# Optimization experiments

Hardware: AMD Instinct MI355X
Metric: run time of the kernel (lower is better)

## Reference

```python
import jax, jax.numpy as jnp
import numpy as np
import math

B, T, C = 4, 2048, 1024
N_HEAD = 16


def setup_inputs() -> dict:
    key = jax.random.key(0)
    ks = jax.random.split(key, 5)
    s = 0.02
    return {
        "x": jax.random.normal(ks[0], (B, T, C), jnp.float32),
        "W_attn": jax.random.normal(ks[1], (C, 3 * C), jnp.float32) * s,
        "b_attn": jax.random.normal(ks[2], (3 * C,), jnp.float32) * s,
        "W_proj": jax.random.normal(ks[3], (C, C), jnp.float32) * s,
        "b_proj": jax.random.normal(ks[4], (C,), jnp.float32) * s,
    }


def reference(x, W_attn, b_attn, W_proj, b_proj):
    b, t, c = x.shape
    hd = c // N_HEAD  # head dim
    qkv = x @ W_attn + b_attn                       # [B,T,3C]
    q, k, v = jnp.split(qkv, 3, axis=-1)
    # [B,T,C] -> [B,H,T,hd]
    q = q.reshape(b, t, N_HEAD, hd).transpose(0, 2, 1, 3)
    k = k.reshape(b, t, N_HEAD, hd).transpose(0, 2, 1, 3)
    v = v.reshape(b, t, N_HEAD, hd).transpose(0, 2, 1, 3)
    att = jnp.einsum("bhqd,bhkd->bhqk", q, k) * (1.0 / math.sqrt(hd))
    causal = jnp.tril(jnp.ones((t, t), dtype=bool))
    att = jnp.where(causal, att, -jnp.inf)
    att = jax.nn.softmax(att, axis=-1)              # dropout disabled (eval mode)
    y = jnp.einsum("bhqk,bhkd->bhqd", att, v)       # [B,H,T,hd]
    y = y.transpose(0, 2, 1, 3).reshape(b, t, c)
    out = y @ W_proj + b_proj                       # resid dropout disabled (eval)
    return out
```

## Files before the change

kernel.cpp:

```cpp
#include <hip/hip_runtime.h>

#define B_  4
#define T_  2048
#define C_  1024
#define H_  16
#define D_  64
#define BT_ 8192

typedef __bf16 bf16x8 __attribute__((ext_vector_type(8)));
typedef float  f32x4  __attribute__((ext_vector_type(4)));

#define MFMA(a, b, c) __builtin_amdgcn_mfma_f32_16x16x32_bf16((a), (b), (c), 0, 0, 0)
#define LOG2E 1.4426950408889634f

__device__ __forceinline__ float fexp2(float x) {
#if __has_builtin(__builtin_amdgcn_exp2f)
    return __builtin_amdgcn_exp2f(x);
#else
    return __expf(x * 0.6931471805599453f);
#endif
}

__device__ __forceinline__ unsigned short f2bf(float f) {
    union { float f; unsigned u; } v; v.f = f;
    unsigned r = v.u + 0x7FFFu + ((v.u >> 16) & 1u);
    return (unsigned short)(r >> 16);
}

__device__ __forceinline__ void gll16(const unsigned short* g, unsigned short* l) {
    __builtin_amdgcn_global_load_lds((const __attribute__((address_space(1))) void*)g,
                                     (__attribute__((address_space(3))) void*)l, 16, 0, 0);
}

template <int GPR>
__device__ __forceinline__ void stage16(const unsigned short* grow0, size_t stride_us,
                                        unsigned short* lds, int chunk) {
    const int lane = threadIdx.x & 63;
    const int gidx = chunk * 64 + lane;
    const int row  = gidx / GPR, c = gidx % GPR;
    const int csrc = c ^ (row & (GPR - 1));
    gll16(grow0 + (size_t)row * stride_us + csrc * 8, lds + gidx * 8);
}

__global__ __launch_bounds__(256) void convert_bf16_kernel(const float* __restrict__ in,
                                                           unsigned short* __restrict__ out) {
    int i = (blockIdx.x * 256 + threadIdx.x) * 4;
    float4 v = *(const float4*)&in[i];
    ushort4 o;
    o.x = f2bf(v.x); o.y = f2bf(v.y); o.z = f2bf(v.z); o.w = f2bf(v.w);
    *(ushort4*)&out[i] = o;
}

__global__ __launch_bounds__(256) void transpose_bf16_kernel(const float* __restrict__ in,
                                                             unsigned short* __restrict__ out,
                                                             int K, int N) {
    __shared__ float tile[32][33];
    int n0 = blockIdx.x * 32, k0 = blockIdx.y * 32;
    int tr = threadIdx.x >> 3, tc = (threadIdx.x & 7) * 4;
    float4 v = *(const float4*)&in[(size_t)(k0 + tr) * N + n0 + tc];
    tile[tr][tc + 0] = v.x; tile[tr][tc + 1] = v.y;
    tile[tr][tc + 2] = v.z; tile[tr][tc + 3] = v.w;
    __syncthreads();
    ushort4 o;
    o.x = f2bf(tile[tc + 0][tr]);
    o.y = f2bf(tile[tc + 1][tr]);
    o.z = f2bf(tile[tc + 2][tr]);
    o.w = f2bf(tile[tc + 3][tr]);
    *(ushort4*)&out[(size_t)(n0 + tr) * K + k0 + tc] = o;
}

__global__ __launch_bounds__(256) void transpose_v_kernel(const unsigned short* __restrict__ qkv,
                                                          unsigned short* __restrict__ vT) {
    __shared__ unsigned short tile[64][65];
    const int bh = blockIdx.y;
    const int b = bh >> 4, h = bh & 15;
    const int t0 = blockIdx.x * 64;
    const size_t src = (size_t)b * 2048 * 3072 + 2048 + h * 64;
    const size_t dbase = (size_t)bh * (T_ * D_);
    const int r = threadIdx.x >> 2, c = (threadIdx.x & 3) * 16;
    uint4 a0 = *(const uint4*)&qkv[src + (size_t)(t0 + r) * 3072 + c];
    uint4 a1 = *(const uint4*)&qkv[src + (size_t)(t0 + r) * 3072 + c + 8];
    const unsigned short* ap = (const unsigned short*)&a0;
    #pragma unroll
    for (int i = 0; i < 8; ++i) tile[r][c + i] = ap[i];
    ap = (const unsigned short*)&a1;
    #pragma unroll
    for (int i = 0; i < 8; ++i) tile[r][c + 8 + i] = ap[i];
    __syncthreads();
    unsigned short tmp[16];
    #pragma unroll
    for (int i = 0; i < 16; ++i) tmp[i] = tile[c + i][r];
    *(uint4*)&vT[dbase + (size_t)r * T_ + t0 + c]     = *(uint4*)&tmp[0];
    *(uint4*)&vT[dbase + (size_t)r * T_ + t0 + c + 8] = *(uint4*)&tmp[8];
}

template <int MODE>
__global__ __launch_bounds__(256) void gemm_bf16_kernel(
    const unsigned short* __restrict__ A,
    const unsigned short* __restrict__ Bt,
    const float* __restrict__ bias,
    float* __restrict__ outF,
    unsigned short* __restrict__ outB,
    int M, int N, int K)
{
    __shared__ __align__(16) unsigned short smem[8192];
    unsigned short* As = smem;
    unsigned short* Bs = smem + 4096;
    const int tid = threadIdx.x;
    const int wave = tid >> 6, lane = tid & 63;
    const int wr = wave >> 1, wc = wave & 1;
    const int g = lane >> 4, li = lane & 15;
    const int m0 = blockIdx.y * 128, n0 = blockIdx.x * 128;

    f32x4 acc[4][4] = {};

    for (int k0 = 0; k0 < K; k0 += 32) {
        __syncthreads();
        stage16<4>(A  + (size_t)m0 * K + k0, K, As, wave * 2);
        stage16<4>(A  + (size_t)m0 * K + k0, K, As, wave * 2 + 1);
        stage16<4>(Bt + (size_t)n0 * K + k0, K, Bs, wave * 2);
        stage16<4>(Bt + (size_t)n0 * K + k0, K, Bs, wave * 2 + 1);
        __syncthreads();
        bf16x8 af[4], bfr[4];
        #pragma unroll
        for (int mi = 0; mi < 4; ++mi) {
            const int row = wr * 64 + mi * 16 + li;
            af[mi] = *(const bf16x8*)&As[row * 32 + ((g ^ (row & 3)) * 8)];
        }
        #pragma unroll
        for (int ni = 0; ni < 4; ++ni) {
            const int row = wc * 64 + ni * 16 + li;
            bfr[ni] = *(const bf16x8*)&Bs[row * 32 + ((g ^ (row & 3)) * 8)];
        }
        #pragma unroll
        for (int mi = 0; mi < 4; ++mi)
            #pragma unroll
            for (int ni = 0; ni < 4; ++ni)
                acc[mi][ni] = MFMA(af[mi], bfr[ni], acc[mi][ni]);
    }

    float bb[4];
    #pragma unroll
    for (int ni = 0; ni < 4; ++ni) bb[ni] = bias[n0 + wc * 64 + ni * 16 + li];

    if (MODE == 0) {
        __syncthreads();
        unsigned short* stg = smem + wave * 1152;
        const float qsc = (n0 < 1024) ? 0.125f * LOG2E : 1.0f;
        const int srow = lane & 15, scp = lane >> 4;
        #pragma unroll
        for (int mi = 0; mi < 4; ++mi) {
            #pragma unroll
            for (int ni = 0; ni < 4; ++ni)
                #pragma unroll
                for (int r = 0; r < 4; ++r)
                    stg[(g * 4 + r) * 72 + ni * 16 + li] = f2bf((acc[mi][ni][r] + bb[ni]) * qsc);
            __builtin_amdgcn_wave_barrier();
            uint4 w0 = *(const uint4*)&stg[srow * 72 + scp * 16];
            uint4 w1 = *(const uint4*)&stg[srow * 72 + scp * 16 + 8];
            unsigned short* dst = &outB[(size_t)(m0 + wr * 64 + mi * 16 + srow) * N
                                        + n0 + wc * 64 + scp * 16];
            *(uint4*)dst = w0;
            *(uint4*)&dst[8] = w1;
            __builtin_amdgcn_wave_barrier();
        }
    } else {
        #pragma unroll
        for (int mi = 0; mi < 4; ++mi)
            #pragma unroll
            for (int ni = 0; ni < 4; ++ni) {
                const int col = n0 + wc * 64 + ni * 16 + li;
                #pragma unroll
                for (int r = 0; r < 4; ++r)
                    outF[(size_t)(m0 + wr * 64 + mi * 16 + g * 4 + r) * N + col]
                        = acc[mi][ni][r] + bb[ni];
            }
    }
}

__global__ __launch_bounds__(256, 4) void flash_attn_kernel(
    const unsigned short* __restrict__ qkv,
    const unsigned short* __restrict__ vT,
    unsigned short* __restrict__ y)
{
    __shared__ __align__(16) unsigned short Ks[64 * 64];
    __shared__ __align__(16) unsigned short Vt[64 * 64];
    __shared__ __align__(16) unsigned short Pq[4][2][16][40];
    const int tid = threadIdx.x;
    const int wv = tid >> 6, lane = tid & 63;
    const int g = lane >> 4, li = lane & 15;
    const int bid = blockIdx.x;
    const int xcd = bid & 7, i = bid >> 3;
    const int bh = xcd * 8 + (i & 7);
    const int p  = i >> 3;
    const int qtA = p, qtB = 31 - p;
    const int b = bh >> 4, h = bh & 15;
    const size_t qrowbase = (size_t)b * 2048 * 3072 + h * 64;
    const size_t vbase = (size_t)bh * (D_ * T_);
    const unsigned short* kbase = qkv + qrowbase + 1024;

    const int rowA = qtA * 64 + wv * 16 + li;
    const int rowB = qtB * 64 + wv * 16 + li;

    bf16x8 aqA[2], aqB[2];
    #pragma unroll
    for (int kc = 0; kc < 2; ++kc) {
        aqA[kc] = *(const bf16x8*)&qkv[qrowbase + (size_t)rowA * 3072 + kc * 32 + g * 8];
        aqB[kc] = *(const bf16x8*)&qkv[qrowbase + (size_t)rowB * 3072 + kc * 32 + g * 8];
    }

    f32x4 oA[4] = {}, oB[4] = {};
    float lA = 0.f, lB = 0.f;
    const float OFS = 8.0f * LOG2E;

    const int nkb = qtB + 1;

    for (int kb = 0; kb < nkb; ++kb) {
        const int k0 = kb << 6;
        __syncthreads();
        stage16<8>(kbase + (size_t)k0 * 3072, 3072, Ks, wv * 2);
        stage16<8>(kbase + (size_t)k0 * 3072, 3072, Ks, wv * 2 + 1);
        stage16<8>(vT + vbase + k0, T_, Vt, wv * 2);
        stage16<8>(vT + vbase + k0, T_, Vt, wv * 2 + 1);
        __syncthreads();
        const bool doA = (kb <= qtA);

        #pragma unroll
        for (int half = 0; half < 2; ++half) {
            f32x4 sA[2], sB[2];
            #pragma unroll
            for (int t2 = 0; t2 < 2; ++t2) {
                const int krow = (half * 2 + t2) * 16 + li;
                bf16x8 ka0 = *(const bf16x8*)&Ks[krow * 64 + ((g       ^ (krow & 7)) * 8)];
                bf16x8 ka1 = *(const bf16x8*)&Ks[krow * 64 + (((4 + g) ^ (krow & 7)) * 8)];
                f32x4 z = {};
                z = MFMA(ka0, aqB[0], z);
                sB[t2] = MFMA(ka1, aqB[1], z);
                if (doA) {
                    f32x4 z2 = {};
                    z2 = MFMA(ka0, aqA[0], z2);
                    sA[t2] = MFMA(ka1, aqA[1], z2);
                }
            }
            #pragma unroll
            for (int t2 = 0; t2 < 2; ++t2) {
                const int kkb = k0 + (half * 2 + t2) * 16;
                {
                    const bool diag = (kb == qtB);
                    ushort4 pw;
                    #pragma unroll
                    for (int r = 0; r < 4; ++r) {
                        float sv = sB[t2][r];
                        if (diag && (kkb + g * 4 + r > rowB)) sv = -1e30f;
                        float pp = fexp2(sv - OFS);
                        lB += pp;
                        ((unsigned short*)&pw)[r] = f2bf(pp);
                    }
                    *(ushort4*)&Pq[wv][1][li][t2 * 16 + g * 4] = pw;
                }
                if (doA) {
                    const bool diag = (kb == qtA);
                    ushort4 pw;
                    #pragma unroll
                    for (int r = 0; r < 4; ++r) {
                        float sv = sA[t2][r];
                        if (diag && (kkb + g * 4 + r > rowA)) sv = -1e30f;
                        float pp = fexp2(sv - OFS);
                        lA += pp;
                        ((unsigned short*)&pw)[r] = f2bf(pp);
                    }
                    *(ushort4*)&Pq[wv][0][li][t2 * 16 + g * 4] = pw;
                }
            }
            __builtin_amdgcn_wave_barrier();
            bf16x8 bpB = *(const bf16x8*)&Pq[wv][1][li][g * 8];
            bf16x8 bpA;
            if (doA) bpA = *(const bf16x8*)&Pq[wv][0][li][g * 8];
            #pragma unroll
            for (int ot = 0; ot < 4; ++ot) {
                const int vrow = ot * 16 + li;
                bf16x8 av = *(const bf16x8*)&Vt[vrow * 64 + (((half * 4 + g) ^ (vrow & 7)) * 8)];
                oB[ot] = MFMA(av, bpB, oB[ot]);
                if (doA) oA[ot] = MFMA(av, bpA, oA[ot]);
            }
            __builtin_amdgcn_wave_barrier();
        }
    }

    #pragma unroll
    for (int t = 0; t < 2; ++t) {
        float l = t ? lB : lA;
        const f32x4* o = t ? oB : oA;
        l += __shfl_xor(l, 16, 64);
        l += __shfl_xor(l, 32, 64);
        float inv = 1.f / l;
        const int trow = (t ? rowB : rowA);
        const size_t yrow = ((size_t)(b * 2048 + trow)) * 1024 + h * 64;
        #pragma unroll
        for (int ot = 0; ot < 4; ++ot) {
            ushort4 pw;
            #pragma unroll
            for (int r = 0; r < 4; ++r)
                ((unsigned short*)&pw)[r] = f2bf(o[ot][r] * inv);
            *(ushort4*)&y[yrow + ot * 16 + g * 4] = pw;
        }
    }
}

extern "C" void kernel_launch(void* const* d_in, const int* in_sizes, int n_in,
                              void* d_out, int out_size, void* d_ws, size_t ws_size,
                              hipStream_t stream)
{
    const float* x      = (const float*)d_in[0];
    const float* W_attn = (const float*)d_in[1];
    const float* b_attn = (const float*)d_in[2];
    const float* W_proj = (const float*)d_in[3];
    const float* b_proj = (const float*)d_in[4];
    float* out = (float*)d_out;

    char* ws = (char*)d_ws;
    size_t off = 0;
    auto alloc = [&](size_t bytes) -> void* {
        void* p = ws + off;
        off += (bytes + 255) & ~(size_t)255;
        return p;
    };
    unsigned short* xb   = (unsigned short*)alloc((size_t)BT_ * C_ * 2);
    unsigned short* Wab  = (unsigned short*)alloc((size_t)3 * C_ * C_ * 2);
    unsigned short* Wpb  = (unsigned short*)alloc((size_t)C_ * C_ * 2);
    unsigned short* qkvb = (unsigned short*)alloc((size_t)BT_ * 3 * C_ * 2);
    unsigned short* yb   = (unsigned short*)alloc((size_t)BT_ * C_ * 2);

    convert_bf16_kernel<<<(BT_ * C_) / 1024, 256, 0, stream>>>(x, xb);
    transpose_bf16_kernel<<<dim3(3 * C_ / 32, C_ / 32), 256, 0, stream>>>(W_attn, Wab, C_, 3 * C_);
    transpose_bf16_kernel<<<dim3(C_ / 32, C_ / 32), 256, 0, stream>>>(W_proj, Wpb, C_, C_);

    gemm_bf16_kernel<0><<<dim3(3 * C_ / 128, BT_ / 128), 256, 0, stream>>>(
        xb, Wab, b_attn, nullptr, qkvb, BT_, 3 * C_, C_);

    unsigned short* vTb = xb;
    transpose_v_kernel<<<dim3(T_ / 64, B_ * H_), 256, 0, stream>>>(qkvb, vTb);

    flash_attn_kernel<<<1024, 256, 0, stream>>>(qkvb, vTb, yb);

    gemm_bf16_kernel<1><<<dim3(C_ / 128, BT_ / 128), 256, 0, stream>>>(
        yb, Wpb, b_proj, out, nullptr, BT_, C_, C_);
}
```

Measured before the change: 279.9 us.

## Fuse prep kernels, write V transposed from QKV GEMM, double-buffer flash K/V

Merges the x conversion and both weight transposes into one launch. The QKV GEMM epilogue now writes V directly in transposed layout when the workspace has room, which removes the separate V-transpose kernel. The flash attention kernel double-buffers its K/V tiles in LDS so the next block's loads overlap the current block's compute, and it shares one P staging buffer between the two query tiles. The trade-offs are more LDS per block, which may reduce occupancy, and extra barriers in the P path.

```diff
diff --git a/kernel.cpp b/kernel.cpp
--- a/kernel.cpp
+++ b/kernel.cpp
@@ -42,21 +42,27 @@
     gll16(grow0 + (size_t)row * stride_us + csrc * 8, lds + gidx * 8);
 }
 
-__global__ __launch_bounds__(256) void convert_bf16_kernel(const float* __restrict__ in,
-                                                           unsigned short* __restrict__ out) {
-    int i = (blockIdx.x * 256 + threadIdx.x) * 4;
-    float4 v = *(const float4*)&in[i];
-    ushort4 o;
-    o.x = f2bf(v.x); o.y = f2bf(v.y); o.z = f2bf(v.z); o.w = f2bf(v.w);
-    *(ushort4*)&out[i] = o;
-}
-
-__global__ __launch_bounds__(256) void transpose_bf16_kernel(const float* __restrict__ in,
-                                                             unsigned short* __restrict__ out,
-                                                             int K, int N) {
+__global__ __launch_bounds__(256) void prep_kernel(const float* __restrict__ x,
+                                                   unsigned short* __restrict__ xb,
+                                                   const float* __restrict__ Wa,
+                                                   unsigned short* __restrict__ Wab,
+                                                   const float* __restrict__ Wp,
+                                                   unsigned short* __restrict__ Wpb) {
     __shared__ float tile[32][33];
-    int n0 = blockIdx.x * 32, k0 = blockIdx.y * 32;
-    int tr = threadIdx.x >> 3, tc = (threadIdx.x & 7) * 4;
+    const int bid = blockIdx.x;
+    if (bid < 8192) {
+        int i = bid * 1024 + threadIdx.x * 4;
+        float4 v = *(const float4*)&x[i];
+        ushort4 o;
+        o.x = f2bf(v.x); o.y = f2bf(v.y); o.z = f2bf(v.z); o.w = f2bf(v.w);
+        *(ushort4*)&xb[i] = o;
+        return;
+    }
+    const float* in; unsigned short* out; int N, t;
+    if (bid < 11264) { t = bid - 8192;  in = Wa; out = Wab; N = 3072; }
+    else             { t = bid - 11264; in = Wp; out = Wpb; N = 1024; }
+    const int n0 = (t % (N / 32)) * 32, k0 = (t / (N / 32)) * 32;
+    const int tr = threadIdx.x >> 3, tc = (threadIdx.x & 7) * 4;
     float4 v = *(const float4*)&in[(size_t)(k0 + tr) * N + n0 + tc];
     tile[tr][tc + 0] = v.x; tile[tr][tc + 1] = v.y;
     tile[tr][tc + 2] = v.z; tile[tr][tc + 3] = v.w;
@@ -66,7 +72,7 @@
     o.y = f2bf(tile[tc + 1][tr]);
     o.z = f2bf(tile[tc + 2][tr]);
     o.w = f2bf(tile[tc + 3][tr]);
-    *(ushort4*)&out[(size_t)(n0 + tr) * K + k0 + tc] = o;
+    *(ushort4*)&out[(size_t)(n0 + tr) * 1024 + k0 + tc] = o;
 }
 
 __global__ __launch_bounds__(256) void transpose_v_kernel(const unsigned short* __restrict__ qkv,
@@ -94,16 +100,17 @@
     *(uint4*)&vT[dbase + (size_t)r * T_ + t0 + c + 8] = *(uint4*)&tmp[8];
 }
 
-template <int MODE>
+template <int MODE, int VDIRECT>
 __global__ __launch_bounds__(256) void gemm_bf16_kernel(
     const unsigned short* __restrict__ A,
     const unsigned short* __restrict__ Bt,
     const float* __restrict__ bias,
     float* __restrict__ outF,
     unsigned short* __restrict__ outB,
+    unsigned short* __restrict__ vTout,
     int M, int N, int K)
 {
-    __shared__ __align__(16) unsigned short smem[8192];
+    __shared__ __align__(16) unsigned short smem[(MODE == 0 && VDIRECT) ? 10240 : 8192];
     unsigned short* As = smem;
     unsigned short* Bs = smem + 4096;
     const int tid = threadIdx.x;
@@ -145,24 +152,54 @@
 
     if (MODE == 0) {
         __syncthreads();
-        unsigned short* stg = smem + wave * 1152;
-        const float qsc = (n0 < 1024) ? 0.125f * LOG2E : 1.0f;
-        const int srow = lane & 15, scp = lane >> 4;
-        #pragma unroll
-        for (int mi = 0; mi < 4; ++mi) {
-            #pragma unroll
-            for (int ni = 0; ni < 4; ++ni)
+        if (VDIRECT && n0 >= 2048) {
+            const int h = (n0 - 2048 + wc * 64) >> 6;
+            const int b = m0 >> 11;
+            const int tb = (m0 & 2047) + wr * 64;
+            unsigned short* vstg = smem + wave * 2560;
+            #pragma unroll
+            for (int mp = 0; mp < 2; ++mp) {
                 #pragma unroll
-                for (int r = 0; r < 4; ++r)
-                    stg[(g * 4 + r) * 72 + ni * 16 + li] = f2bf((acc[mi][ni][r] + bb[ni]) * qsc);
-            __builtin_amdgcn_wave_barrier();
-            uint4 w0 = *(const uint4*)&stg[srow * 72 + scp * 16];
-            uint4 w1 = *(const uint4*)&stg[srow * 72 + scp * 16 + 8];
-            unsigned short* dst = &outB[(size_t)(m0 + wr * 64 + mi * 16 + srow) * N
-                                        + n0 + wc * 64 + scp * 16];
-            *(uint4*)dst = w0;
-            *(uint4*)&dst[8] = w1;
-            __builtin_amdgcn_wave_barrier();
+                for (int mh = 0; mh < 2; ++mh) {
+                    const int mi = mp * 2 + mh;
+                    #pragma unroll
+                    for (int ni = 0; ni < 4; ++ni)
+                        #pragma unroll
+                        for (int r = 0; r < 4; ++r)
+                            vstg[(ni * 16 + li) * 40 + mh * 16 + g * 4 + r]
+                                = f2bf(acc[mi][ni][r] + bb[ni]);
+                }
+                __builtin_amdgcn_wave_barrier();
+                uint4 w0 = *(const uint4*)&vstg[lane * 40];
+                uint4 w1 = *(const uint4*)&vstg[lane * 40 + 8];
+                uint4 w2 = *(const uint4*)&vstg[lane * 40 + 16];
+                uint4 w3 = *(const uint4*)&vstg[lane * 40 + 24];
+                unsigned short* dp = vTout
+                    + (((size_t)(b * 16 + h) * 64 + lane) * 2048 + tb + mp * 32);
+                *(uint4*)dp = w0; *(uint4*)&dp[8] = w1;
+                *(uint4*)&dp[16] = w2; *(uint4*)&dp[24] = w3;
+                __builtin_amdgcn_wave_barrier();
+            }
+        } else {
+            unsigned short* stg = smem + wave * 1152;
+            const float qsc = (n0 < 1024) ? 0.125f * LOG2E : 1.0f;
+            const int srow = lane & 15, scp = lane >> 4;
+            #pragma unroll
+            for (int mi = 0; mi < 4; ++mi) {
+                #pragma unroll
+                for (int ni = 0; ni < 4; ++ni)
+                    #pragma unroll
+                    for (int r = 0; r < 4; ++r)
+                        stg[(g * 4 + r) * 72 + ni * 16 + li] = f2bf((acc[mi][ni][r] + bb[ni]) * qsc);
+                __builtin_amdgcn_wave_barrier();
+                uint4 w0 = *(const uint4*)&stg[srow * 72 + scp * 16];
+                uint4 w1 = *(const uint4*)&stg[srow * 72 + scp * 16 + 8];
+                unsigned short* dst = &outB[(size_t)(m0 + wr * 64 + mi * 16 + srow) * N
+                                            + n0 + wc * 64 + scp * 16];
+                *(uint4*)dst = w0;
+                *(uint4*)&dst[8] = w1;
+                __builtin_amdgcn_wave_barrier();
+            }
         }
     } else {
         #pragma unroll
@@ -183,9 +220,9 @@
     const unsigned short* __restrict__ vT,
     unsigned short* __restrict__ y)
 {
-    __shared__ __align__(16) unsigned short Ks[64 * 64];
-    __shared__ __align__(16) unsigned short Vt[64 * 64];
-    __shared__ __align__(16) unsigned short Pq[4][2][16][40];
+    __shared__ __align__(16) unsigned short Ks[2][64 * 64];
+    __shared__ __align__(16) unsigned short Vt[2][64 * 64];
+    __shared__ __align__(16) unsigned short Pq[4][16][40];
     const int tid = threadIdx.x;
     const int wv = tid >> 6, lane = tid & 63;
     const int g = lane >> 4, li = lane & 15;
@@ -212,18 +249,28 @@
     f32x4 oA[4] = {}, oB[4] = {};
     float lA = 0.f, lB = 0.f;
     const float OFS = 8.0f * LOG2E;
-
     const int nkb = qtB + 1;
 
+    stage16<8>(kbase, 3072, Ks[0], wv * 2);
+    stage16<8>(kbase, 3072, Ks[0], wv * 2 + 1);
+    stage16<8>(vT + vbase, T_, Vt[0], wv * 2);
+    stage16<8>(vT + vbase, T_, Vt[0], wv * 2 + 1);
+
     for (int kb = 0; kb < nkb; ++kb) {
+        const int cur = kb & 1;
+        __syncthreads();
+        if (kb + 1 < nkb) {
+            const int kn = (kb + 1) << 6;
+            const int nxt = cur ^ 1;
+            stage16<8>(kbase + (size_t)kn * 3072, 3072, Ks[nxt], wv * 2);
+            stage16<8>(kbase + (size_t)kn * 3072, 3072, Ks[nxt], wv * 2 + 1);
+            stage16<8>(vT + vbase + kn, T_, Vt[nxt], wv * 2);
+            stage16<8>(vT + vbase + kn, T_, Vt[nxt], wv * 2 + 1);
+        }
         const int k0 = kb << 6;
-        __syncthreads();
-        stage16<8>(kbase + (size_t)k0 * 3072, 3072, Ks, wv * 2);
-        stage16<8>(kbase + (size_t)k0 * 3072, 3072, Ks, wv * 2 + 1);
-        stage16<8>(vT + vbase + k0, T_, Vt, wv * 2);
-        stage16<8>(vT + vbase + k0, T_, Vt, wv * 2 + 1);
-        __syncthreads();
         const bool doA = (kb <= qtA);
+        const unsigned short* ksb = Ks[cur];
+        const unsigned short* vtb = Vt[cur];
 
         #pragma unroll
         for (int half = 0; half < 2; ++half) {
@@ -231,8 +278,8 @@
             #pragma unroll
             for (int t2 = 0; t2 < 2; ++t2) {
                 const int krow = (half * 2 + t2) * 16 + li;
-                bf16x8 ka0 = *(const bf16x8*)&Ks[krow * 64 + ((g       ^ (krow & 7)) * 8)];
-                bf16x8 ka1 = *(const bf16x8*)&Ks[krow * 64 + (((4 + g) ^ (krow & 7)) * 8)];
+                bf16x8 ka0 = *(const bf16x8*)&ksb[krow * 64 + ((g       ^ (krow & 7)) * 8)];
+                bf16x8 ka1 = *(const bf16x8*)&ksb[krow * 64 + (((4 + g) ^ (krow & 7)) * 8)];
                 f32x4 z = {};
                 z = MFMA(ka0, aqB[0], z);
                 sB[t2] = MFMA(ka1, aqB[1], z);
@@ -242,10 +289,11 @@
                     sA[t2] = MFMA(ka1, aqA[1], z2);
                 }
             }
-            #pragma unroll
-            for (int t2 = 0; t2 < 2; ++t2) {
-                const int kkb = k0 + (half * 2 + t2) * 16;
-                {
+            bf16x8 bpA, bpB;
+            {
+                #pragma unroll
+                for (int t2 = 0; t2 < 2; ++t2) {
+                    const int kkb = k0 + (half * 2 + t2) * 16;
                     const bool diag = (kb == qtB);
                     ushort4 pw;
                     #pragma unroll
@@ -256,9 +304,16 @@
                         lB += pp;
                         ((unsigned short*)&pw)[r] = f2bf(pp);
                     }
-                    *(ushort4*)&Pq[wv][1][li][t2 * 16 + g * 4] = pw;
+                    *(ushort4*)&Pq[wv][li][t2 * 16 + g * 4] = pw;
                 }
-                if (doA) {
+                __builtin_amdgcn_wave_barrier();
+                bpB = *(const bf16x8*)&Pq[wv][li][g * 8];
+                __builtin_amdgcn_wave_barrier();
+            }
+            if (doA) {
+                #pragma unroll
+                for (int t2 = 0; t2 < 2; ++t2) {
+                    const int kkb = k0 + (half * 2 + t2) * 16;
                     const bool diag = (kb == qtA);
                     ushort4 pw;
                     #pragma unroll
@@ -269,17 +324,16 @@
                         lA += pp;
                         ((unsigned short*)&pw)[r] = f2bf(pp);
                     }
-                    *(ushort4*)&Pq[wv][0][li][t2 * 16 + g * 4] = pw;
+                    *(ushort4*)&Pq[wv][li][t2 * 16 + g * 4] = pw;
                 }
-            }
-            __builtin_amdgcn_wave_barrier();
-            bf16x8 bpB = *(const bf16x8*)&Pq[wv][1][li][g * 8];
-            bf16x8 bpA;
-            if (doA) bpA = *(const bf16x8*)&Pq[wv][0][li][g * 8];
+                __builtin_amdgcn_wave_barrier();
+                bpA = *(const bf16x8*)&Pq[wv][li][g * 8];
+                __builtin_amdgcn_wave_barrier();
+            }
             #pragma unroll
             for (int ot = 0; ot < 4; ++ot) {
                 const int vrow = ot * 16 + li;
-                bf16x8 av = *(const bf16x8*)&Vt[vrow * 64 + (((half * 4 + g) ^ (vrow & 7)) * 8)];
+                bf16x8 av = *(const bf16x8*)&vtb[vrow * 64 + (((half * 4 + g) ^ (vrow & 7)) * 8)];
                 oB[ot] = MFMA(av, bpB, oB[ot]);
                 if (doA) oA[ot] = MFMA(av, bpA, oA[ot]);
             }
@@ -330,19 +384,24 @@
     unsigned short* Wpb  = (unsigned short*)alloc((size_t)C_ * C_ * 2);
     unsigned short* qkvb = (unsigned short*)alloc((size_t)BT_ * 3 * C_ * 2);
     unsigned short* yb   = (unsigned short*)alloc((size_t)BT_ * C_ * 2);
-
-    convert_bf16_kernel<<<(BT_ * C_) / 1024, 256, 0, stream>>>(x, xb);
-    transpose_bf16_kernel<<<dim3(3 * C_ / 32, C_ / 32), 256, 0, stream>>>(W_attn, Wab, C_, 3 * C_);
-    transpose_bf16_kernel<<<dim3(C_ / 32, C_ / 32), 256, 0, stream>>>(W_proj, Wpb, C_, C_);
-
-    gemm_bf16_kernel<0><<<dim3(3 * C_ / 128, BT_ / 128), 256, 0, stream>>>(
-        xb, Wab, b_attn, nullptr, qkvb, BT_, 3 * C_, C_);
-
-    unsigned short* vTb = xb;
-    transpose_v_kernel<<<dim3(T_ / 64, B_ * H_), 256, 0, stream>>>(qkvb, vTb);
+    const size_t vt_bytes = (size_t)BT_ * C_ * 2;
+    const bool vdirect = (ws_size >= off + vt_bytes);
+    unsigned short* vTb = vdirect ? (unsigned short*)alloc(vt_bytes)
+                                  : xb;
+
+    prep_kernel<<<12288, 256, 0, stream>>>(x, xb, W_attn, Wab, W_proj, Wpb);
+
+    if (vdirect) {
+        gemm_bf16_kernel<0, 1><<<dim3(24, 64), 256, 0, stream>>>(
+            xb, Wab, b_attn, nullptr, qkvb, vTb, BT_, 3 * C_, C_);
+    } else {
+        gemm_bf16_kernel<0, 0><<<dim3(24, 64), 256, 0, stream>>>(
+            xb, Wab, b_attn, nullptr, qkvb, nullptr, BT_, 3 * C_, C_);
+        transpose_v_kernel<<<dim3(T_ / 64, B_ * H_), 256, 0, stream>>>(qkvb, vTb);
+    }
 
     flash_attn_kernel<<<1024, 256, 0, stream>>>(qkvb, vTb, yb);
 
-    gemm_bf16_kernel<1><<<dim3(C_ / 128, BT_ / 128), 256, 0, stream>>>(
-        yb, Wpb, b_proj, out, nullptr, BT_, C_, C_);
-}
+    gemm_bf16_kernel<1, 0><<<dim3(8, 64), 256, 0, stream>>>(
+        yb, Wpb, b_proj, out, nullptr, nullptr, BT_, C_, C_);
+}
```

After: 265.8 us. 5.0% less time.
